# Kernel optimization log

Hardware: AMD Instinct MI355X
Metric: run time of the kernel (lower is better)

Reference implementation:

```python
import jax, jax.numpy as jnp
import numpy as np

N_NODES = 50000
N_EDGES = 1000000
IN_C = 128
HID_C = 128
N_REL = 8


def rgcn_conv(x, W, root, b, src, dst, et, n_rel):
    # PyG-style RGCNConv: per-relation linear transform of source features,
    # mean-aggregated per (target node, relation), plus root transform + bias.
    n = x.shape[0]
    h = jnp.einsum('nd,rdh->nrh', x, W)          # [N, R, H] per-relation transforms
    msgs = h[src, et]                            # [E, H] gather per-edge message
    seg = dst * n_rel + et                       # combined (node, relation) segment id
    agg = jax.ops.segment_sum(msgs, seg, num_segments=n * n_rel)        # [N*R, H]
    cnt = jax.ops.segment_sum(jnp.ones_like(msgs[:, 0]), seg, num_segments=n * n_rel)
    agg = agg / jnp.maximum(cnt, 1.0)[:, None]   # mean over edges of each relation
    return agg.reshape(n, n_rel, -1).sum(axis=1) + x @ root + b


def setup_inputs() -> dict:
    key = jax.random.key(0)
    ks = jax.random.split(key, 12)
    s = 1.0 / np.sqrt(IN_C)
    sh = 1.0 / np.sqrt(HID_C)
    return {
        'x': jax.random.normal(ks[0], (N_NODES, IN_C), dtype=jnp.float32),
        'ei': jax.random.randint(ks[1], (2, N_EDGES), 0, N_NODES, dtype=jnp.int32),
        'et': jax.random.randint(ks[2], (N_EDGES,), 0, N_REL, dtype=jnp.int32),
        'W1': jax.random.normal(ks[3], (N_REL, IN_C, HID_C), dtype=jnp.float32) * s,
        'root1': jax.random.normal(ks[4], (IN_C, HID_C), dtype=jnp.float32) * s,
        'b1': jnp.zeros((HID_C,), dtype=jnp.float32),
        'W2': jax.random.normal(ks[5], (N_REL, HID_C, HID_C), dtype=jnp.float32) * sh,
        'root2': jax.random.normal(ks[6], (HID_C, HID_C), dtype=jnp.float32) * sh,
        'b2': jnp.zeros((HID_C,), dtype=jnp.float32),
        'lin_W': jax.random.normal(ks[7], (HID_C, HID_C), dtype=jnp.float32) * sh,
        'lin_b': jnp.zeros((HID_C,), dtype=jnp.float32),
    }


def reference(x, ei, et, W1, root1, b1, W2, root2, b2, lin_W, lin_b):
    src, dst = ei[0], ei[1]
    h = jax.nn.relu(rgcn_conv(x, W1, root1, b1, src, dst, et, N_REL))
    h = rgcn_conv(h, W2, root2, b2, src, dst, et, N_REL)
    return h @ lin_W + lin_b
```

## Files before the change

### kernel.cpp

```cpp
#include <hip/hip_runtime.h>
#include <hip/hip_bf16.h>

#define N_NODES 50000
#define N_EDGES 1000000
#define C       128
#define N_REL   8
#define N_SEG   (N_NODES * N_REL)
#define KTOT    (N_REL * C + C)
#define KC_CNT  (KTOT / 32)
#define A_STRIDE 1160
#define NCHUNK  ((N_SEG + 1023) / 1024)
#define MV_N    (N_SEG + 1 + N_EDGES)
#define NBLK    (N_NODES / 16)
#define FE_BLK  ((N_EDGES + 511) / 512)

typedef __hip_bfloat16  bf16;
typedef __hip_bfloat162 bf162;
typedef __attribute__((ext_vector_type(8))) short short8;
typedef __attribute__((ext_vector_type(4))) float f32x4;

__device__ __forceinline__ size_t frag_index(int k, int n) {
    int nt = n >> 4, n15 = n & 15;
    int kc = k >> 5, quad = (k >> 3) & 3, j = k & 7;
    int lane = quad * 16 + n15;
    return ((size_t)(nt * KC_CNT + kc) * 64 + lane) * 8 + j;
}

#define CVT_BLOCKS ((N_NODES * C / 2) / 256)
#define CNT_BLOCKS ((N_EDGES + 255) / 256)
__global__ void prep_kernel(const float2* __restrict__ xf, unsigned int* __restrict__ xb,
                            const int* __restrict__ dst, const int* __restrict__ et,
                            int* __restrict__ cnt, int* __restrict__ rank) {
    int bid = blockIdx.x;
    if (bid < CVT_BLOCKS) {
        int i = bid * 256 + threadIdx.x;
        float2 v = xf[i];
        union { bf162 h; unsigned int u; } cv;
        cv.h = bf162(__float2bfloat16(v.x), __float2bfloat16(v.y));
        xb[i] = cv.u;
    } else {
        int e = (bid - CVT_BLOCKS) * 256 + threadIdx.x;
        if (e < N_EDGES) rank[e] = atomicAdd(&cnt[dst[e] * N_REL + et[e]], 1);
    }
}

#define RP_B  (KTOT * C / 256)
#define RPT_B ((KTOT / 16) * (C / 16))
__global__ void scanA_kernel(const int* __restrict__ cnt, int* __restrict__ offs,
                             int* __restrict__ partials,
                             const float* __restrict__ W1, const float* __restrict__ root1,
                             const float* __restrict__ W2, const float* __restrict__ root2,
                             const float* __restrict__ linW,
                             const float* __restrict__ b2, const float* __restrict__ linb,
                             bf16* __restrict__ Bp1, bf16* __restrict__ Bp2,
                             float* __restrict__ b2p) {
    int bid = blockIdx.x;
    int t   = threadIdx.x;
    if (bid < NCHUNK) {
        __shared__ int tot[256];
        int base = bid * 1024 + t * 4;
        int v0 = (base + 0 < N_SEG) ? cnt[base + 0] : 0;
        int v1 = (base + 1 < N_SEG) ? cnt[base + 1] : 0;
        int v2 = (base + 2 < N_SEG) ? cnt[base + 2] : 0;
        int v3 = (base + 3 < N_SEG) ? cnt[base + 3] : 0;
        int tsum = v0 + v1 + v2 + v3;
        tot[t] = tsum;
        __syncthreads();
        for (int d = 1; d < 256; d <<= 1) {
            int x = tot[t];
            int y = (t >= d) ? tot[t - d] : 0;
            __syncthreads();
            tot[t] = x + y;
            __syncthreads();
        }
        int excl = tot[t] - tsum;
        if (base + 0 < N_SEG) offs[base + 0] = excl;
        if (base + 1 < N_SEG) offs[base + 1] = excl + v0;
        if (base + 2 < N_SEG) offs[base + 2] = excl + v0 + v1;
        if (base + 3 < N_SEG) offs[base + 3] = excl + v0 + v1 + v2;
        if (t == 255) partials[bid] = tot[255];
    } else if (bid < NCHUNK + RP_B) {
        int idx = (bid - NCHUNK) * 256 + t;
        int k = idx >> 7, n = idx & 127;
        float val;
        if (k < N_REL * C) val = W1[(size_t)k * C + n];
        else               val = root1[(size_t)(k - N_REL * C) * C + n];
        Bp1[frag_index(k, n)] = __float2bfloat16(val);
    } else if (bid < NCHUNK + RP_B + RPT_B) {
        __shared__ float Wt[16][128];
        __shared__ float Lt[128][16];
        int tileid = bid - NCHUNK - RP_B;
        int kt = tileid >> 3;
        int n0 = (tileid & 7) * 16;
        int k0 = kt * 16;
        const float* baseW = (k0 < N_REL * C) ? (W2 + (size_t)k0 * C)
                                              : (root2 + (size_t)(k0 - N_REL * C) * C);
#pragma unroll
        for (int r = 0; r < 8; r++) {
            int idx = t + r * 256;
            Wt[idx >> 7][idx & 127] = baseW[idx];
        }
#pragma unroll
        for (int r = 0; r < 8; r++) {
            int idx = t + r * 256;
            Lt[idx >> 4][idx & 15] = linW[(size_t)(idx >> 4) * C + n0 + (idx & 15)];
        }
        __syncthreads();
        int ty = t >> 4, tx = t & 15;
        float acc = 0.f;
#pragma unroll 8
        for (int m = 0; m < 128; m++)
            acc += Wt[ty][m] * Lt[m][tx];
        Bp2[frag_index(k0 + ty, n0 + tx)] = __float2bfloat16(acc);
    } else {
        if (t < 128) {
            float acc = linb[t];
            for (int m = 0; m < C; m++)
                acc += b2[m] * linW[(size_t)m * C + t];
            b2p[t] = acc;
        }
    }
}

__global__ void fillB_kernel(const int* __restrict__ src, const int* __restrict__ dst,
                             const int* __restrict__ et,
                             const int* __restrict__ offs_raw,
                             const int* __restrict__ partials,
                             const int* __restrict__ rank,
                             int* __restrict__ srcs_out,
                             int* __restrict__ spx) {
    __shared__ int s[512];
    int t = threadIdx.x;
    int bid = blockIdx.x;
    s[t] = (t < NCHUNK) ? partials[t] : 0;
    __syncthreads();
    for (int d = 1; d < 512; d <<= 1) {
        int x = s[t];
        int y = (t >= d) ? s[t - d] : 0;
        __syncthreads();
        s[t] = x + y;
        __syncthreads();
    }
    if (bid == 0 && t < NCHUNK) spx[t] = (t == 0) ? 0 : s[t - 1];
    int e = bid * 512 + t;
    if (e < N_EDGES) {
        int seg = dst[e] * N_REL + et[e];
        int chunk = seg >> 10;
        int base = offs_raw[seg] + ((chunk == 0) ? 0 : s[chunk - 1]);
        srcs_out[base + rank[e]] = src[e];
    }
}

template <int RELU, int OUT_F32, int COPY_CSR, int RAWOFFS>
__global__ __launch_bounds__(512, 6) void fused_layer(
        const unsigned int* __restrict__ featu,
        const int*   __restrict__ offs,
        const int*   __restrict__ srcs,
        const short8* __restrict__ Bp,
        const float* __restrict__ bias,
        void* __restrict__ outp,
        int* __restrict__ offs2, int* __restrict__ srcs2,
        const int* __restrict__ spx)
{
    __shared__ __align__(16) unsigned int At[16 * (A_STRIDE / 2)];
    __shared__ int offsL[129];
    const int tid  = threadIdx.x;
    const int lane = tid & 63;
    const int w    = tid >> 6;
    const int v0   = blockIdx.x * 16;

    if (tid < 129) {
        int idx = v0 * 8 + tid;
        int val;
        if (RAWOFFS) val = (idx < N_SEG) ? offs[idx] + spx[idx >> 10] : N_EDGES;
        else         val = offs[idx];
        offsL[tid] = val;
    }
    if (tid < 64)  At[(tid >> 2) * (A_STRIDE / 2) + 576 + (tid & 3)] = 0u;

    if (COPY_CSR) {
        for (int i = blockIdx.x * 512 + tid; i < MV_N; i += NBLK * 512) {
            if (i < N_SEG + 1) {
                int val;
                if (RAWOFFS) val = (i < N_SEG) ? offs[i] + spx[i >> 10] : N_EDGES;
                else         val = offs[i];
                offs2[i] = val;
            } else {
                srcs2[i - (N_SEG + 1)] = srcs[i - (N_SEG + 1)];
            }
        }
    }

    for (int q = tid; q < 16 * 64; q += 512) {
        int node = q >> 6, pch = q & 63;
        At[node * (A_STRIDE / 2) + 512 + pch] = featu[(size_t)(v0 + node) * 64 + pch];
    }
    __syncthreads();

    {
        const int segLo = w * 16;
        const int segHi = segLo + 16;
        int curSeg = segLo;
        int segEnd = offsL[curSeg + 1];
        int i      = offsL[segLo];
        const int eend = offsL[segHi];
        float a0 = 0.f, a1 = 0.f;

        unsigned int vals[16];
        bool have = (i + 16 <= eend);
        if (have) {
            const int ib = __builtin_amdgcn_readfirstlane(i);
            int sv[16];
#pragma unroll
            for (int j = 0; j < 16; j++) sv[j] = srcs[ib + j];
#pragma unroll
            for (int j = 0; j < 16; j++) vals[j] = featu[(size_t)sv[j] * 64 + lane];
        }
        while (have) {
            const int inext = i + 16;
            const bool havenext = (inext + 16 <= eend);
            unsigned int vals2[16];
            if (havenext) {
                const int ib2 = __builtin_amdgcn_readfirstlane(inext);
                int sv2[16];
#pragma unroll
                for (int j = 0; j < 16; j++) sv2[j] = srcs[ib2 + j];
#pragma unroll
                for (int j = 0; j < 16; j++) vals2[j] = featu[(size_t)sv2[j] * 64 + lane];
            }
#pragma unroll
            for (int j = 0; j < 16; j++) {
                while (i + j == segEnd) {
                    int b = offsL[curSeg];
                    float inv = (segEnd > b) ? 1.0f / (float)(segEnd - b) : 0.0f;
                    union { bf162 h; unsigned int u; } cv;
                    cv.h = bf162(__float2bfloat16(a0 * inv), __float2bfloat16(a1 * inv));
                    At[(curSeg >> 3) * (A_STRIDE / 2) + (curSeg & 7) * 64 + lane] = cv.u;
                    a0 = 0.f; a1 = 0.f;
                    curSeg++;
                    segEnd = offsL[curSeg + 1];
                }
                union { bf162 h; unsigned int u; } uv; uv.u = vals[j];
                a0 += __low2float(uv.h);
                a1 += __high2float(uv.h);
            }
            i = inext;
            have = havenext;
            if (havenext) {
#pragma unroll
                for (int j = 0; j < 16; j++) vals[j] = vals2[j];
            }
        }
        {
            int m = eend - i;
            const int ib = __builtin_amdgcn_readfirstlane(i);
            int sv[16];
#pragma unroll
            for (int j = 0; j < 16; j++) if (j < m) sv[j] = srcs[ib + j];
            unsigned int tvals[16];
#pragma unroll
            for (int j = 0; j < 16; j++) if (j < m) tvals[j] = featu[(size_t)sv[j] * 64 + lane];
#pragma unroll
            for (int j = 0; j < 16; j++) {
                if (j < m) {
                    while (i + j == segEnd) {
                        int b = offsL[curSeg];
                        float inv = (segEnd > b) ? 1.0f / (float)(segEnd - b) : 0.0f;
                        union { bf162 h; unsigned int u; } cv;
                        cv.h = bf162(__float2bfloat16(a0 * inv), __float2bfloat16(a1 * inv));
                        At[(curSeg >> 3) * (A_STRIDE / 2) + (curSeg & 7) * 64 + lane] = cv.u;
                        a0 = 0.f; a1 = 0.f;
                        curSeg++;
                        segEnd = offsL[curSeg + 1];
                    }
                    union { bf162 h; unsigned int u; } uv; uv.u = tvals[j];
                    a0 += __low2float(uv.h);
                    a1 += __high2float(uv.h);
                }
            }
        }
        while (curSeg < segHi) {
            int b = offsL[curSeg], e2 = offsL[curSeg + 1];
            float inv = (e2 > b) ? 1.0f / (float)(e2 - b) : 0.0f;
            union { bf162 h; unsigned int u; } cv;
            cv.h = bf162(__float2bfloat16(a0 * inv), __float2bfloat16(a1 * inv));
            At[(curSeg >> 3) * (A_STRIDE / 2) + (curSeg & 7) * 64 + lane] = cv.u;
            a0 = 0.f; a1 = 0.f;
            curSeg++;
        }
    }
    __syncthreads();

    const int quad = lane >> 4, n15 = lane & 15;
    f32x4 acc = {0.f, 0.f, 0.f, 0.f};
    const short* Ash = (const short*)At;

    short8 b0 = Bp[(size_t)(w * KC_CNT) * 64 + lane];
#pragma unroll 4
    for (int kc = 0; kc < KC_CNT; kc++) {
        short8 cb0 = b0;
        if (kc + 1 < KC_CNT)
            b0 = Bp[(size_t)(w * KC_CNT + kc + 1) * 64 + lane];
        short8 a = *reinterpret_cast<const short8*>(Ash + n15 * A_STRIDE + kc * 32 + quad * 8);
        acc = __builtin_amdgcn_mfma_f32_16x16x32_bf16(a, cb0, acc, 0, 0, 0);
    }

    {
        int col = w * 16 + n15;
        float bv = bias[col];
#pragma unroll
        for (int r = 0; r < 4; r++) {
            int m = quad * 4 + r;
            float v = acc[r] + bv;
            if (RELU) v = fmaxf(v, 0.f);
            if (OUT_F32) ((float*)outp)[(size_t)(v0 + m) * C + col] = v;
            else         ((bf16*)outp)[(size_t)(v0 + m) * C + col] = __float2bfloat16(v);
        }
    }
}

extern "C" void kernel_launch(void* const* d_in, const int* in_sizes, int n_in,
                              void* d_out, int out_size, void* d_ws, size_t ws_size,
                              hipStream_t stream) {
    const float* x     = (const float*)d_in[0];
    const int*   ei    = (const int*)d_in[1];
    const int*   et    = (const int*)d_in[2];
    const float* W1    = (const float*)d_in[3];
    const float* root1 = (const float*)d_in[4];
    const float* b1    = (const float*)d_in[5];
    const float* W2    = (const float*)d_in[6];
    const float* root2 = (const float*)d_in[7];
    const float* b2    = (const float*)d_in[8];
    const float* linW  = (const float*)d_in[9];
    const float* linb  = (const float*)d_in[10];
    const int* src = ei;
    const int* dst = ei + N_EDGES;

    char* ob = (char*)d_out;
    int* cnt_i    = (int*)(ob + 0);
    int* offs_t   = (int*)(ob + 1600000);
    int* partials = (int*)(ob + 3200000);
    int* spx      = (int*)(ob + 3201792);
    int* srcs_t   = (int*)(ob + 3203584);
    int* rank     = (int*)(ob + 7203584);
    unsigned int* xb16 = (unsigned int*)(ob + 11203584);

    char* eb = (char*)d_in[1];
    int* offs2 = (int*)(eb + 0);
    int* srcs2 = (int*)(eb + 1600256);

    char* xbuf = (char*)d_in[0];
    unsigned int* h1 = (unsigned int*)xbuf;
    bf16*  Bp1 = (bf16*)(xbuf + 13000192);
    bf16*  Bp2 = (bf16*)(xbuf + 13295360);
    float* b2p = (float*)(xbuf + 13590528);

    float* out = (float*)d_out;

    hipMemsetAsync(cnt_i, 0, 1600000, stream);
    prep_kernel<<<CVT_BLOCKS + CNT_BLOCKS, 256, 0, stream>>>(
        (const float2*)x, xb16, dst, et, cnt_i, rank);
    scanA_kernel<<<NCHUNK + RP_B + RPT_B + 1, 256, 0, stream>>>(
        cnt_i, offs_t, partials, W1, root1, W2, root2, linW, b2, linb,
        Bp1, Bp2, b2p);
    fillB_kernel<<<FE_BLK, 512, 0, stream>>>(
        src, dst, et, offs_t, partials, rank, srcs_t, spx);

    fused_layer<1, 0, 1, 1><<<NBLK, 512, 0, stream>>>(
        xb16, offs_t, srcs_t, (const short8*)Bp1, b1, (void*)h1, offs2, srcs2, spx);
    fused_layer<0, 1, 0, 0><<<NBLK, 512, 0, stream>>>(
        h1, offs2, srcs2, (const short8*)Bp2, b2p, (void*)out, nullptr, nullptr, nullptr);

    (void)in_sizes; (void)n_in; (void)out_size; (void)d_ws; (void)ws_size;
}
```

Baseline: 296.8 us.

## Merge CSR build and both layers into two cooperative persistent kernels

Replaces the memset, prep, scan, fill kernels and the two layer launches with two cooperative kernels that use grid-wide syncs between phases. The build kernel zeroes counts, converts x, counts edges, scans, packs weights and scatters sources, and packs rank and segment into a single word so the scatter pass no longer rereads dst and et. The fused kernel runs both layers as persistent tile loops with a grid sync between them. The aim is to remove launch gaps and tail effects. The cost is grid-sync overhead, persistent blocks with reduced occupancy, and a 13-bit limit on per-segment rank.

```diff
diff --git a/kernel.cpp b/kernel.cpp
--- a/kernel.cpp
+++ b/kernel.cpp
@@ -1,5 +1,8 @@
 #include <hip/hip_runtime.h>
 #include <hip/hip_bf16.h>
+#include <hip/hip_cooperative_groups.h>
+
+namespace cg = cooperative_groups;
 
 #define N_NODES 50000
 #define N_EDGES 1000000
@@ -12,7 +15,9 @@
 #define NCHUNK  ((N_SEG + 1023) / 1024)
 #define MV_N    (N_SEG + 1 + N_EDGES)
 #define NBLK    (N_NODES / 16)
-#define FE_BLK  ((N_EDGES + 511) / 512)
+#define RPB1    (KTOT * C / 512)
+#define RPT_B   ((KTOT / 16) * (C / 16))
+#define P2_VB   (NCHUNK + RPB1 + RPT_B + 1)
 
 typedef __hip_bfloat16  bf16;
 typedef __hip_bfloat162 bf162;
@@ -26,148 +31,147 @@
     return ((size_t)(nt * KC_CNT + kc) * 64 + lane) * 8 + j;
 }
 
-#define CVT_BLOCKS ((N_NODES * C / 2) / 256)
-#define CNT_BLOCKS ((N_EDGES + 255) / 256)
-__global__ void prep_kernel(const float2* __restrict__ xf, unsigned int* __restrict__ xb,
-                            const int* __restrict__ dst, const int* __restrict__ et,
-                            int* __restrict__ cnt, int* __restrict__ rank) {
-    int bid = blockIdx.x;
-    if (bid < CVT_BLOCKS) {
-        int i = bid * 256 + threadIdx.x;
+__global__ __launch_bounds__(512, 8) void build_kernel(
+        const float2* __restrict__ xf, unsigned int* __restrict__ xb,
+        const int* __restrict__ src, const int* __restrict__ dst, const int* __restrict__ et,
+        int* __restrict__ cnt, int* __restrict__ rankseg,
+        int* __restrict__ offs, int* __restrict__ partials, int* __restrict__ spx,
+        const float* __restrict__ W1, const float* __restrict__ root1,
+        const float* __restrict__ W2, const float* __restrict__ root2,
+        const float* __restrict__ linW, const float* __restrict__ b2v,
+        const float* __restrict__ linb,
+        bf16* __restrict__ Bp1, bf16* __restrict__ Bp2, float* __restrict__ b2p,
+        int* __restrict__ srcs_out)
+{
+    cg::grid_group gg = cg::this_grid();
+    __shared__ __align__(16) char smem[16384];
+    const int t = threadIdx.x, bid = blockIdx.x, nb = gridDim.x;
+    const int gtid = bid * 512 + t, gstr = nb * 512;
+
+    for (int i = gtid; i < N_SEG; i += gstr) cnt[i] = 0;
+    for (int i = gtid; i < N_NODES * C / 2; i += gstr) {
         float2 v = xf[i];
         union { bf162 h; unsigned int u; } cv;
         cv.h = bf162(__float2bfloat16(v.x), __float2bfloat16(v.y));
         xb[i] = cv.u;
-    } else {
-        int e = (bid - CVT_BLOCKS) * 256 + threadIdx.x;
-        if (e < N_EDGES) rank[e] = atomicAdd(&cnt[dst[e] * N_REL + et[e]], 1);
+    }
+    gg.sync();
+
+    for (int e = gtid; e < N_EDGES; e += gstr) {
+        int seg = dst[e] * N_REL + et[e];
+        int r = atomicAdd(&cnt[seg], 1);
+        rankseg[e] = (r << 19) | seg;
+    }
+    gg.sync();
+
+    {
+        int* tot = (int*)smem;
+        for (int vb = bid; vb < P2_VB; vb += nb) {
+            if (vb < NCHUNK) {
+                int base = vb * 1024 + t * 2;
+                int v0 = (base < N_SEG) ? cnt[base] : 0;
+                int v1 = (base + 1 < N_SEG) ? cnt[base + 1] : 0;
+                int ts = v0 + v1;
+                tot[t] = ts;
+                __syncthreads();
+                for (int d = 1; d < 512; d <<= 1) {
+                    int x = tot[t];
+                    int y = (t >= d) ? tot[t - d] : 0;
+                    __syncthreads();
+                    tot[t] = x + y;
+                    __syncthreads();
+                }
+                int excl = tot[t] - ts;
+                if (base < N_SEG)     offs[base]     = excl;
+                if (base + 1 < N_SEG) offs[base + 1] = excl + v0;
+                if (t == 511) partials[vb] = tot[511];
+            } else if (vb < NCHUNK + RPB1) {
+                int idx = (vb - NCHUNK) * 512 + t;
+                int k = idx >> 7, n = idx & 127;
+                float val;
+                if (k < N_REL * C) val = W1[(size_t)k * C + n];
+                else               val = root1[(size_t)(k - N_REL * C) * C + n];
+                Bp1[frag_index(k, n)] = __float2bfloat16(val);
+            } else if (vb < NCHUNK + RPB1 + RPT_B) {
+                float (*Wt)[128] = (float (*)[128])smem;
+                float (*Lt)[16]  = (float (*)[16])(smem + 8192);
+                int tileid = vb - NCHUNK - RPB1;
+                int kt = tileid >> 3;
+                int n0 = (tileid & 7) * 16;
+                int k0 = kt * 16;
+                const float* baseW = (k0 < N_REL * C) ? (W2 + (size_t)k0 * C)
+                                                      : (root2 + (size_t)(k0 - N_REL * C) * C);
+#pragma unroll
+                for (int r = 0; r < 4; r++) {
+                    int idx = t + r * 512;
+                    Wt[idx >> 7][idx & 127] = baseW[idx];
+                }
+#pragma unroll
+                for (int r = 0; r < 4; r++) {
+                    int idx = t + r * 512;
+                    Lt[idx >> 4][idx & 15] = linW[(size_t)(idx >> 4) * C + n0 + (idx & 15)];
+                }
+                __syncthreads();
+                if (t < 256) {
+                    int ty = t >> 4, tx = t & 15;
+                    float acc = 0.f;
+#pragma unroll 8
+                    for (int m = 0; m < 128; m++)
+                        acc += Wt[ty][m] * Lt[m][tx];
+                    Bp2[frag_index(k0 + ty, n0 + tx)] = __float2bfloat16(acc);
+                }
+            } else {
+                if (t < 128) {
+                    float acc = linb[t];
+                    for (int m = 0; m < C; m++)
+                        acc += b2v[m] * linW[(size_t)m * C + t];
+                    b2p[t] = acc;
+                }
+            }
+            __syncthreads();
+        }
+    }
+    gg.sync();
+
+    {
+        int* s = (int*)smem;
+        s[t] = (t < NCHUNK) ? partials[t] : 0;
+        __syncthreads();
+        for (int d = 1; d < 512; d <<= 1) {
+            int x = s[t];
+            int y = (t >= d) ? s[t - d] : 0;
+            __syncthreads();
+            s[t] = x + y;
+            __syncthreads();
+        }
+        if (bid == 0 && t < NCHUNK) spx[t] = (t == 0) ? 0 : s[t - 1];
+        for (int e = gtid; e < N_EDGES; e += gstr) {
+            int rs = rankseg[e];
+            int seg = rs & 0x7FFFF;
+            int r = ((unsigned int)rs) >> 19;
+            int chunk = seg >> 10;
+            int base = offs[seg] + ((chunk == 0) ? 0 : s[chunk - 1]);
+            srcs_out[base + r] = src[e];
+        }
     }
 }
 
-#define RP_B  (KTOT * C / 256)
-#define RPT_B ((KTOT / 16) * (C / 16))
-__global__ void scanA_kernel(const int* __restrict__ cnt, int* __restrict__ offs,
-                             int* __restrict__ partials,
-                             const float* __restrict__ W1, const float* __restrict__ root1,
-                             const float* __restrict__ W2, const float* __restrict__ root2,
-                             const float* __restrict__ linW,
-                             const float* __restrict__ b2, const float* __restrict__ linb,
-                             bf16* __restrict__ Bp1, bf16* __restrict__ Bp2,
-                             float* __restrict__ b2p) {
-    int bid = blockIdx.x;
-    int t   = threadIdx.x;
-    if (bid < NCHUNK) {
-        __shared__ int tot[256];
-        int base = bid * 1024 + t * 4;
-        int v0 = (base + 0 < N_SEG) ? cnt[base + 0] : 0;
-        int v1 = (base + 1 < N_SEG) ? cnt[base + 1] : 0;
-        int v2 = (base + 2 < N_SEG) ? cnt[base + 2] : 0;
-        int v3 = (base + 3 < N_SEG) ? cnt[base + 3] : 0;
-        int tsum = v0 + v1 + v2 + v3;
-        tot[t] = tsum;
-        __syncthreads();
-        for (int d = 1; d < 256; d <<= 1) {
-            int x = tot[t];
-            int y = (t >= d) ? tot[t - d] : 0;
-            __syncthreads();
-            tot[t] = x + y;
-            __syncthreads();
-        }
-        int excl = tot[t] - tsum;
-        if (base + 0 < N_SEG) offs[base + 0] = excl;
-        if (base + 1 < N_SEG) offs[base + 1] = excl + v0;
-        if (base + 2 < N_SEG) offs[base + 2] = excl + v0 + v1;
-        if (base + 3 < N_SEG) offs[base + 3] = excl + v0 + v1 + v2;
-        if (t == 255) partials[bid] = tot[255];
-    } else if (bid < NCHUNK + RP_B) {
-        int idx = (bid - NCHUNK) * 256 + t;
-        int k = idx >> 7, n = idx & 127;
-        float val;
-        if (k < N_REL * C) val = W1[(size_t)k * C + n];
-        else               val = root1[(size_t)(k - N_REL * C) * C + n];
-        Bp1[frag_index(k, n)] = __float2bfloat16(val);
-    } else if (bid < NCHUNK + RP_B + RPT_B) {
-        __shared__ float Wt[16][128];
-        __shared__ float Lt[128][16];
-        int tileid = bid - NCHUNK - RP_B;
-        int kt = tileid >> 3;
-        int n0 = (tileid & 7) * 16;
-        int k0 = kt * 16;
-        const float* baseW = (k0 < N_REL * C) ? (W2 + (size_t)k0 * C)
-                                              : (root2 + (size_t)(k0 - N_REL * C) * C);
-#pragma unroll
-        for (int r = 0; r < 8; r++) {
-            int idx = t + r * 256;
-            Wt[idx >> 7][idx & 127] = baseW[idx];
-        }
-#pragma unroll
-        for (int r = 0; r < 8; r++) {
-            int idx = t + r * 256;
-            Lt[idx >> 4][idx & 15] = linW[(size_t)(idx >> 4) * C + n0 + (idx & 15)];
-        }
-        __syncthreads();
-        int ty = t >> 4, tx = t & 15;
-        float acc = 0.f;
-#pragma unroll 8
-        for (int m = 0; m < 128; m++)
-            acc += Wt[ty][m] * Lt[m][tx];
-        Bp2[frag_index(k0 + ty, n0 + tx)] = __float2bfloat16(acc);
-    } else {
-        if (t < 128) {
-            float acc = linb[t];
-            for (int m = 0; m < C; m++)
-                acc += b2[m] * linW[(size_t)m * C + t];
-            b2p[t] = acc;
-        }
-    }
-}
-
-__global__ void fillB_kernel(const int* __restrict__ src, const int* __restrict__ dst,
-                             const int* __restrict__ et,
-                             const int* __restrict__ offs_raw,
-                             const int* __restrict__ partials,
-                             const int* __restrict__ rank,
-                             int* __restrict__ srcs_out,
-                             int* __restrict__ spx) {
-    __shared__ int s[512];
-    int t = threadIdx.x;
-    int bid = blockIdx.x;
-    s[t] = (t < NCHUNK) ? partials[t] : 0;
-    __syncthreads();
-    for (int d = 1; d < 512; d <<= 1) {
-        int x = s[t];
-        int y = (t >= d) ? s[t - d] : 0;
-        __syncthreads();
-        s[t] = x + y;
-        __syncthreads();
-    }
-    if (bid == 0 && t < NCHUNK) spx[t] = (t == 0) ? 0 : s[t - 1];
-    int e = bid * 512 + t;
-    if (e < N_EDGES) {
-        int seg = dst[e] * N_REL + et[e];
-        int chunk = seg >> 10;
-        int base = offs_raw[seg] + ((chunk == 0) ? 0 : s[chunk - 1]);
-        srcs_out[base + rank[e]] = src[e];
-    }
-}
-
-template <int RELU, int OUT_F32, int COPY_CSR, int RAWOFFS>
-__global__ __launch_bounds__(512, 6) void fused_layer(
+template <int RELU, int OUT_F32, int RAWOFFS>
+__device__ __forceinline__ void layer_tile(
+        int tileid,
         const unsigned int* __restrict__ featu,
         const int*   __restrict__ offs,
         const int*   __restrict__ srcs,
         const short8* __restrict__ Bp,
         const float* __restrict__ bias,
         void* __restrict__ outp,
-        int* __restrict__ offs2, int* __restrict__ srcs2,
-        const int* __restrict__ spx)
+        const int* __restrict__ spx,
+        unsigned int* At, int* offsL)
 {
-    __shared__ __align__(16) unsigned int At[16 * (A_STRIDE / 2)];
-    __shared__ int offsL[129];
     const int tid  = threadIdx.x;
     const int lane = tid & 63;
     const int w    = tid >> 6;
-    const int v0   = blockIdx.x * 16;
+    const int v0   = tileid * 16;
 
     if (tid < 129) {
         int idx = v0 * 8 + tid;
@@ -177,19 +181,6 @@
         offsL[tid] = val;
     }
     if (tid < 64)  At[(tid >> 2) * (A_STRIDE / 2) + 576 + (tid & 3)] = 0u;
-
-    if (COPY_CSR) {
-        for (int i = blockIdx.x * 512 + tid; i < MV_N; i += NBLK * 512) {
-            if (i < N_SEG + 1) {
-                int val;
-                if (RAWOFFS) val = (i < N_SEG) ? offs[i] + spx[i >> 10] : N_EDGES;
-                else         val = offs[i];
-                offs2[i] = val;
-            } else {
-                srcs2[i - (N_SEG + 1)] = srcs[i - (N_SEG + 1)];
-            }
-        }
-    }
 
     for (int q = tid; q < 16 * 64; q += 512) {
         int node = q >> 6, pch = q & 63;
@@ -317,6 +308,36 @@
             else         ((bf16*)outp)[(size_t)(v0 + m) * C + col] = __float2bfloat16(v);
         }
     }
+    __syncthreads();
+}
+
+__global__ __launch_bounds__(512, 8) void fused2_kernel(
+        const unsigned int* __restrict__ xb16,
+        const int* __restrict__ offs_raw, const int* __restrict__ srcs_t,
+        const short8* __restrict__ Bp1, const float* __restrict__ b1,
+        unsigned int* __restrict__ h1,
+        int* __restrict__ offs2, int* __restrict__ srcs2,
+        const int* __restrict__ spx,
+        const short8* __restrict__ Bp2, const float* __restrict__ b2p,
+        float* __restrict__ out)
+{
+    cg::grid_group gg = cg::this_grid();
+    __shared__ __align__(16) unsigned int At[16 * (A_STRIDE / 2)];
+    __shared__ int offsL[129];
+    const int bid = blockIdx.x, nb = gridDim.x, tid = threadIdx.x;
+
+    for (int i = bid * 512 + tid; i < MV_N; i += nb * 512) {
+        if (i < N_SEG + 1) offs2[i] = (i < N_SEG) ? offs_raw[i] + spx[i >> 10] : N_EDGES;
+        else               srcs2[i - (N_SEG + 1)] = srcs_t[i - (N_SEG + 1)];
+    }
+
+    for (int tile = bid; tile < NBLK; tile += nb)
+        layer_tile<1, 0, 1>(tile, xb16, offs_raw, srcs_t, Bp1, b1, (void*)h1, spx, At, offsL);
+
+    gg.sync();
+
+    for (int tile = bid; tile < NBLK; tile += nb)
+        layer_tile<0, 1, 0>(tile, h1, offs2, srcs2, Bp2, b2p, (void*)out, nullptr, At, offsL);
 }
 
 extern "C" void kernel_launch(void* const* d_in, const int* in_sizes, int n_in,
@@ -342,7 +363,7 @@
     int* partials = (int*)(ob + 3200000);
     int* spx      = (int*)(ob + 3201792);
     int* srcs_t   = (int*)(ob + 3203584);
-    int* rank     = (int*)(ob + 7203584);
+    int* rankseg  = (int*)(ob + 7203584);
     unsigned int* xb16 = (unsigned int*)(ob + 11203584);
 
     char* eb = (char*)d_in[1];
@@ -357,19 +378,45 @@
 
     float* out = (float*)d_out;
 
-    hipMemsetAsync(cnt_i, 0, 1600000, stream);
-    prep_kernel<<<CVT_BLOCKS + CNT_BLOCKS, 256, 0, stream>>>(
-        (const float2*)x, xb16, dst, et, cnt_i, rank);
-    scanA_kernel<<<NCHUNK + RP_B + RPT_B + 1, 256, 0, stream>>>(
-        cnt_i, offs_t, partials, W1, root1, W2, root2, linW, b2, linb,
-        Bp1, Bp2, b2p);
-    fillB_kernel<<<FE_BLK, 512, 0, stream>>>(
-        src, dst, et, offs_t, partials, rank, srcs_t, spx);
-
-    fused_layer<1, 0, 1, 1><<<NBLK, 512, 0, stream>>>(
-        xb16, offs_t, srcs_t, (const short8*)Bp1, b1, (void*)h1, offs2, srcs2, spx);
-    fused_layer<0, 1, 0, 0><<<NBLK, 512, 0, stream>>>(
-        h1, offs2, srcs2, (const short8*)Bp2, b2p, (void*)out, nullptr, nullptr, nullptr);
+    static int gridB = 0, gridF = 0;
+    if (gridF == 0) {
+        int dev = 0;
+        hipGetDevice(&dev);
+        hipDeviceProp_t prop;
+        hipGetDeviceProperties(&prop, dev);
+        int nCU = prop.multiProcessorCount;
+        if (nCU <= 0) nCU = 256;
+        int occB = 0, occF = 0;
+        hipOccupancyMaxActiveBlocksPerMultiprocessor(&occB, (const void*)build_kernel, 512, 0);
+        hipOccupancyMaxActiveBlocksPerMultiprocessor(&occF, (const void*)fused2_kernel, 512, 0);
+        if (occB < 1) occB = 1;
+        if (occF < 1) occF = 1;
+        gridB = occB * nCU;
+        if (gridB > 2048) gridB = 2048;
+        int maxF = occF * nCU;
+        int tpb  = (NBLK + maxF - 1) / maxF;
+        gridF = (NBLK + tpb - 1) / tpb;
+    }
+
+    const float2* xf = (const float2*)x;
+    void* argsB[] = {
+        (void*)&xf, (void*)&xb16, (void*)&src, (void*)&dst, (void*)&et,
+        (void*)&cnt_i, (void*)&rankseg, (void*)&offs_t, (void*)&partials, (void*)&spx,
+        (void*)&W1, (void*)&root1, (void*)&W2, (void*)&root2, (void*)&linW,
+        (void*)&b2, (void*)&linb, (void*)&Bp1, (void*)&Bp2, (void*)&b2p,
+        (void*)&srcs_t };
+    hipLaunchCooperativeKernel((const void*)build_kernel, dim3(gridB), dim3(512),
+                               argsB, 0, stream);
+
+    const short8* Bp1v = (const short8*)Bp1;
+    const short8* Bp2v = (const short8*)Bp2;
+    void* argsF[] = {
+        (void*)&xb16, (void*)&offs_t, (void*)&srcs_t,
+        (void*)&Bp1v, (void*)&b1, (void*)&h1,
+        (void*)&offs2, (void*)&srcs2, (void*)&spx,
+        (void*)&Bp2v, (void*)&b2p, (void*)&out };
+    hipLaunchCooperativeKernel((const void*)fused2_kernel, dim3(gridF), dim3(512),
+                               argsF, 0, stream);
 
     (void)in_sizes; (void)n_in; (void)out_size; (void)d_ws; (void)ws_size;
 }
```

Measured after the change: 655.3 us. +120.8%, slower.

## Build final CSR once in fillB into input buffers, drop layer-1 CSR copy

Applied to the files above, without the earlier changes.

fillB now writes the fully scanned offsets and the sorted source list straight into reused input buffers (the dst half of ei and the et array), so layer 1 no longer copies the CSR for layer 2 and both layers read the same final arrays. prep packs rank and segment into one int, so fillB reads one array instead of dst, et and rank. The x-to-bf16 conversion is widened to float4 loads. This removes roughly 7 MB of extra CSR copy traffic and a scattered read pass, at the cost of overwriting input buffers (dst and et are consumed before they are overwritten) and a bit-packing limit of 2^19 segments with 13-bit ranks.

```diff
diff --git a/kernel.cpp b/kernel.cpp
--- a/kernel.cpp
+++ b/kernel.cpp
@@ -10,7 +10,6 @@
 #define KC_CNT  (KTOT / 32)
 #define A_STRIDE 1160
 #define NCHUNK  ((N_SEG + 1023) / 1024)
-#define MV_N    (N_SEG + 1 + N_EDGES)
 #define NBLK    (N_NODES / 16)
 #define FE_BLK  ((N_EDGES + 511) / 512)
 
@@ -26,21 +25,28 @@
     return ((size_t)(nt * KC_CNT + kc) * 64 + lane) * 8 + j;
 }
 
-#define CVT_BLOCKS ((N_NODES * C / 2) / 256)
+#define CVT_BLOCKS ((N_NODES * C / 4) / 256)
 #define CNT_BLOCKS ((N_EDGES + 255) / 256)
-__global__ void prep_kernel(const float2* __restrict__ xf, unsigned int* __restrict__ xb,
+typedef __attribute__((ext_vector_type(2))) unsigned int uint2v;
+__global__ void prep_kernel(const float4* __restrict__ xf, uint2v* __restrict__ xb,
                             const int* __restrict__ dst, const int* __restrict__ et,
-                            int* __restrict__ cnt, int* __restrict__ rank) {
+                            int* __restrict__ cnt, int* __restrict__ rankseg) {
     int bid = blockIdx.x;
     if (bid < CVT_BLOCKS) {
         int i = bid * 256 + threadIdx.x;
-        float2 v = xf[i];
-        union { bf162 h; unsigned int u; } cv;
-        cv.h = bf162(__float2bfloat16(v.x), __float2bfloat16(v.y));
-        xb[i] = cv.u;
+        float4 v = xf[i];
+        union { bf162 h; unsigned int u; } c0, c1;
+        c0.h = bf162(__float2bfloat16(v.x), __float2bfloat16(v.y));
+        c1.h = bf162(__float2bfloat16(v.z), __float2bfloat16(v.w));
+        uint2v o; o.x = c0.u; o.y = c1.u;
+        xb[i] = o;
     } else {
         int e = (bid - CVT_BLOCKS) * 256 + threadIdx.x;
-        if (e < N_EDGES) rank[e] = atomicAdd(&cnt[dst[e] * N_REL + et[e]], 1);
+        if (e < N_EDGES) {
+            int seg = dst[e] * N_REL + et[e];
+            int r = atomicAdd(&cnt[seg], 1);
+            rankseg[e] = (r << 19) | seg;
+        }
     }
 }
 
@@ -122,13 +128,12 @@
     }
 }
 
-__global__ void fillB_kernel(const int* __restrict__ src, const int* __restrict__ dst,
-                             const int* __restrict__ et,
+__global__ void fillB_kernel(const int* __restrict__ src,
+                             const int* __restrict__ rankseg,
                              const int* __restrict__ offs_raw,
                              const int* __restrict__ partials,
-                             const int* __restrict__ rank,
                              int* __restrict__ srcs_out,
-                             int* __restrict__ spx) {
+                             int* __restrict__ offs_final) {
     __shared__ int s[512];
     int t = threadIdx.x;
     int bid = blockIdx.x;
@@ -141,26 +146,31 @@
         s[t] = x + y;
         __syncthreads();
     }
-    if (bid == 0 && t < NCHUNK) spx[t] = (t == 0) ? 0 : s[t - 1];
     int e = bid * 512 + t;
+    if (e < N_SEG) {
+        int chunk = e >> 10;
+        offs_final[e] = offs_raw[e] + ((chunk == 0) ? 0 : s[chunk - 1]);
+    } else if (e == N_SEG) {
+        offs_final[N_SEG] = N_EDGES;
+    }
     if (e < N_EDGES) {
-        int seg = dst[e] * N_REL + et[e];
+        int rs = rankseg[e];
+        int seg = rs & 0x7FFFF;
+        int r = ((unsigned int)rs) >> 19;
         int chunk = seg >> 10;
         int base = offs_raw[seg] + ((chunk == 0) ? 0 : s[chunk - 1]);
-        srcs_out[base + rank[e]] = src[e];
-    }
-}
-
-template <int RELU, int OUT_F32, int COPY_CSR, int RAWOFFS>
+        srcs_out[base + r] = src[e];
+    }
+}
+
+template <int RELU, int OUT_F32>
 __global__ __launch_bounds__(512, 6) void fused_layer(
         const unsigned int* __restrict__ featu,
         const int*   __restrict__ offs,
         const int*   __restrict__ srcs,
         const short8* __restrict__ Bp,
         const float* __restrict__ bias,
-        void* __restrict__ outp,
-        int* __restrict__ offs2, int* __restrict__ srcs2,
-        const int* __restrict__ spx)
+        void* __restrict__ outp)
 {
     __shared__ __align__(16) unsigned int At[16 * (A_STRIDE / 2)];
     __shared__ int offsL[129];
@@ -169,27 +179,8 @@
     const int w    = tid >> 6;
     const int v0   = blockIdx.x * 16;
 
-    if (tid < 129) {
-        int idx = v0 * 8 + tid;
-        int val;
-        if (RAWOFFS) val = (idx < N_SEG) ? offs[idx] + spx[idx >> 10] : N_EDGES;
-        else         val = offs[idx];
-        offsL[tid] = val;
-    }
+    if (tid < 129) offsL[tid] = offs[v0 * 8 + tid];
     if (tid < 64)  At[(tid >> 2) * (A_STRIDE / 2) + 576 + (tid & 3)] = 0u;
-
-    if (COPY_CSR) {
-        for (int i = blockIdx.x * 512 + tid; i < MV_N; i += NBLK * 512) {
-            if (i < N_SEG + 1) {
-                int val;
-                if (RAWOFFS) val = (i < N_SEG) ? offs[i] + spx[i >> 10] : N_EDGES;
-                else         val = offs[i];
-                offs2[i] = val;
-            } else {
-                srcs2[i - (N_SEG + 1)] = srcs[i - (N_SEG + 1)];
-            }
-        }
-    }
 
     for (int q = tid; q < 16 * 64; q += 512) {
         int node = q >> 6, pch = q & 63;
@@ -340,14 +331,11 @@
     int* cnt_i    = (int*)(ob + 0);
     int* offs_t   = (int*)(ob + 1600000);
     int* partials = (int*)(ob + 3200000);
-    int* spx      = (int*)(ob + 3201792);
-    int* srcs_t   = (int*)(ob + 3203584);
-    int* rank     = (int*)(ob + 7203584);
-    unsigned int* xb16 = (unsigned int*)(ob + 11203584);
-
-    char* eb = (char*)d_in[1];
-    int* offs2 = (int*)(eb + 0);
-    int* srcs2 = (int*)(eb + 1600256);
+    int* rankseg  = (int*)(ob + 3203584);
+    unsigned int* xb16 = (unsigned int*)(ob + 7203584);
+
+    int* srcs_f = (int*)((char*)d_in[1] + 4000000);
+    int* offs_f = (int*)d_in[2];
 
     char* xbuf = (char*)d_in[0];
     unsigned int* h1 = (unsigned int*)xbuf;
@@ -359,17 +347,17 @@
 
     hipMemsetAsync(cnt_i, 0, 1600000, stream);
     prep_kernel<<<CVT_BLOCKS + CNT_BLOCKS, 256, 0, stream>>>(
-        (const float2*)x, xb16, dst, et, cnt_i, rank);
+        (const float4*)x, (uint2v*)xb16, dst, et, cnt_i, rankseg);
     scanA_kernel<<<NCHUNK + RP_B + RPT_B + 1, 256, 0, stream>>>(
         cnt_i, offs_t, partials, W1, root1, W2, root2, linW, b2, linb,
         Bp1, Bp2, b2p);
     fillB_kernel<<<FE_BLK, 512, 0, stream>>>(
-        src, dst, et, offs_t, partials, rank, srcs_t, spx);
-
-    fused_layer<1, 0, 1, 1><<<NBLK, 512, 0, stream>>>(
-        xb16, offs_t, srcs_t, (const short8*)Bp1, b1, (void*)h1, offs2, srcs2, spx);
-    fused_layer<0, 1, 0, 0><<<NBLK, 512, 0, stream>>>(
-        h1, offs2, srcs2, (const short8*)Bp2, b2p, (void*)out, nullptr, nullptr, nullptr);
+        src, rankseg, offs_t, partials, srcs_f, offs_f);
+
+    fused_layer<1, 0><<<NBLK, 512, 0, stream>>>(
+        xb16, offs_f, srcs_f, (const short8*)Bp1, b1, (void*)h1);
+    fused_layer<0, 1><<<NBLK, 512, 0, stream>>>(
+        h1, offs_f, srcs_f, (const short8*)Bp2, b2p, (void*)out);
 
     (void)in_sizes; (void)n_in; (void)out_size; (void)d_ws; (void)ws_size;
 }
```

Result: no change. 291.9 us (-1.7%).
